# Kernel tuning notes

Hardware: AMD Instinct MI355X
Metric: run time of the kernel (lower is better)

Reference implementation:

```python
import math
import jax, jax.numpy as jnp
import numpy as np

HEAD_SIZE = 64
MAX_LEN = 1024
ENT_HEADS = 2
REL_HEADS = 24
NEG_BIG = 1e12


def rope_tables(max_pos=MAX_LEN, head_size=HEAD_SIZE):
    # coord_dim=2 -> table built with d_hid = head_size // 2
    d = head_size // 2
    pos = jnp.arange(max_pos, dtype=jnp.float32)[:, None]            # [P,1]
    div = jnp.exp(jnp.arange(0, d, 2, dtype=jnp.float32) * (-math.log(10000.0) / d))  # [d/2]
    ang = pos * div                                                   # [P, d/2]
    # table[:,1::2]=cos, table[:,::2]=sin; repeat_interleave(2) == jnp.repeat(...,2)
    cosp = jnp.repeat(jnp.cos(ang), 2, axis=-1)                       # [P, d]
    sinp = jnp.repeat(jnp.sin(ang), 2, axis=-1)                       # [P, d]
    return cosp, sinp


def apply_rope2d(qw, cosp, sinp, xp, yp):
    # qw: [b,s,h,hs]; xp,yp: [b,s] int positions
    cos = jnp.concatenate([cosp[xp], cosp[yp]], axis=-1)[:, :, None, :]  # [b,s,1,hs]
    sin = jnp.concatenate([sinp[xp], sinp[yp]], axis=-1)[:, :, None, :]
    qw2 = jnp.stack([-qw[..., 1::2], qw[..., ::2]], axis=-1).reshape(qw.shape)
    return qw * cos + qw2 * sin


def gp_layer(x, W, b, heads, mask, xp, yp, cosp, sinp, tril):
    hs = HEAD_SIZE
    bsz, s, _ = x.shape
    # dense then torch.chunk(heads)+stack == reshape to [b,s,heads,2*hs]
    seq = (x @ W + b).reshape(bsz, s, heads, 2 * hs)
    qw, kw = seq[..., :hs], seq[..., hs:]
    qw = apply_rope2d(qw, cosp, sinp, xp, yp)
    kw = apply_rope2d(kw, cosp, sinp, xp, yp)
    logits = jnp.einsum('bmhd,bnhd->bhmn', qw, kw)                    # [b,h,s,s]
    pad = (mask[:, None, :, None] > 0) & (mask[:, None, None, :] > 0)
    logits = jnp.where(pad, logits, -jnp.inf)
    if tril:
        logits = logits - jnp.tril(jnp.ones((s, s), logits.dtype), -1) * NEG_BIG
    return logits / (hs ** 0.5)


def setup_inputs() -> dict:
    key = jax.random.key(0)
    ks = jax.random.split(key, 8)
    b, s, h = 4, 512, 1024
    return {
        'last_hidden_state': jax.random.normal(ks[0], (b, s, h), dtype=jnp.float32),
        'attention_mask': jnp.ones((b, s), dtype=jnp.int32),
        'x_pos': jax.random.randint(ks[1], (b, s), 0, MAX_LEN, dtype=jnp.int32),
        'y_pos': jax.random.randint(ks[2], (b, s), 0, MAX_LEN, dtype=jnp.int32),
        'W_ent': jax.random.normal(ks[3], (h, ENT_HEADS * 2 * HEAD_SIZE), dtype=jnp.float32) * 0.02,
        'b_ent': jnp.zeros((ENT_HEADS * 2 * HEAD_SIZE,), dtype=jnp.float32),
        'W_head': jax.random.normal(ks[4], (h, REL_HEADS * 2 * HEAD_SIZE), dtype=jnp.float32) * 0.02,
        'b_head': jnp.zeros((REL_HEADS * 2 * HEAD_SIZE,), dtype=jnp.float32),
        'W_tail': jax.random.normal(ks[5], (h, REL_HEADS * 2 * HEAD_SIZE), dtype=jnp.float32) * 0.02,
        'b_tail': jnp.zeros((REL_HEADS * 2 * HEAD_SIZE,), dtype=jnp.float32),
    }


def reference(last_hidden_state, attention_mask, x_pos, y_pos,
              W_ent, b_ent, W_head, b_head, W_tail, b_tail):
    cosp, sinp = rope_tables()
    ent = gp_layer(last_hidden_state, W_ent, b_ent, ENT_HEADS,
                   attention_mask, x_pos, y_pos, cosp, sinp, tril=True)
    head = gp_layer(last_hidden_state, W_head, b_head, REL_HEADS,
                    attention_mask, x_pos, y_pos, cosp, sinp, tril=False)
    tail = gp_layer(last_hidden_state, W_tail, b_tail, REL_HEADS,
                    attention_mask, x_pos, y_pos, cosp, sinp, tril=False)
    return jnp.concatenate([ent, head, tail], axis=1)  # [b, 2+24+24, s, s]
```

## Files before the change

### kernel.cpp

```cpp
#include <hip/hip_runtime.h>
#include <hip/hip_bf16.h>
#include <math.h>

#define NUM_B 4
#define SEQ 512
#define HID 1024
#define NH 50
#define NCOL 6400
#define M_TOK 2048

typedef short bf16x8_t __attribute__((ext_vector_type(8)));
typedef float f32x4_t __attribute__((ext_vector_type(4)));

__device__ __forceinline__ unsigned short f2bf(float f) {
    union { float f; unsigned int u; } v; v.f = f;
    unsigned int u = v.u;
    u += 0x7fffu + ((u >> 16) & 1u);
    return (unsigned short)(u >> 16);
}

__device__ __forceinline__ void gload_lds16(const void* g, void* l) {
    __builtin_amdgcn_global_load_lds(
        (__attribute__((address_space(1))) unsigned int*)(unsigned long long)g,
        (__attribute__((address_space(3))) unsigned int*)(unsigned long long)(uintptr_t)l,
        16, 0, 0);
}

__global__ void k_prep(const float* __restrict__ x, unsigned short* __restrict__ xb,
                       float2* __restrict__ csT,
                       const float* __restrict__ be, const float* __restrict__ bh,
                       const float* __restrict__ bt, float* __restrict__ ball) {
    int bid = blockIdx.x, tid = threadIdx.x;
    if (bid < 2048) {
        int i = bid * 256 + tid;
        float4 v = ((const float4*)x)[i];
        ushort4 o;
        o.x = f2bf(v.x); o.y = f2bf(v.y); o.z = f2bf(v.z); o.w = f2bf(v.w);
        ((ushort4*)xb)[i] = o;
    } else if (bid < 2112) {
        int idx = (bid - 2048) * 256 + tid;
        int p = idx >> 4, t2 = idx & 15;
        float ang = (float)p * expf(-logf(10000.f) * (float)(2 * t2) / 32.f);
        csT[idx] = make_float2(cosf(ang), sinf(ang));
    } else {
        int i = (bid - 2112) * 256 + tid;
        if (i < 6400) {
            float v;
            if (i < 256) v = be[i];
            else if (i < 3328) v = bh[i - 256];
            else v = bt[i - 3328];
            ball[i] = v;
        }
    }
}

__global__ void k_cvt_w(const float* __restrict__ We, const float* __restrict__ Wh,
                        const float* __restrict__ Wl, unsigned short* __restrict__ Wo) {
    __shared__ float t[32][33];
    int n = blockIdx.x * 32 + threadIdx.x;
    const float* W; int Nw, nc;
    if (n < 256)       { W = We; Nw = 256;  nc = n; }
    else if (n < 3328) { W = Wh; Nw = 3072; nc = n - 256; }
    else               { W = Wl; Nw = 3072; nc = n - 3328; }
    int k = blockIdx.y * 32 + threadIdx.y;
    t[threadIdx.y][threadIdx.x] = W[(size_t)k * Nw + nc];
    __syncthreads();
    int on = blockIdx.x * 32 + threadIdx.y;
    int ok = blockIdx.y * 32 + threadIdx.x;
    Wo[(size_t)on * HID + ok] = f2bf(t[threadIdx.x][threadIdx.y]);
}

#define FUSED_LDS_BYTES (144 * 1024)

__global__ __launch_bounds__(512, 2) void k_fused(const unsigned short* __restrict__ xb,
                                                  const unsigned short* __restrict__ Wt,
                                                  const float* __restrict__ bias,
                                                  const int* __restrict__ xp,
                                                  const int* __restrict__ yp,
                                                  const float2* __restrict__ csT,
                                                  const int* __restrict__ mask,
                                                  float* __restrict__ out) {
    extern __shared__ unsigned short smem[];
    unsigned short* As = smem;
    unsigned short* Bs = smem + 512 * 64;
    unsigned short* Qs = smem;
    unsigned short* Ks = smem + 640 * 64;

    int tid = threadIdx.x;
    int wave = tid >> 6, lane = tid & 63;
    int l15 = lane & 15, q = lane >> 4;
    int bh = blockIdx.x;
    int b = bh / NH, h = bh - b * NH;

    const unsigned short* Ab = xb + (size_t)b * SEQ * HID;
    const unsigned short* Bb = Wt + (size_t)h * 128 * HID;

    f32x4_t acc[8][4];
#pragma unroll
    for (int i = 0; i < 8; i++)
#pragma unroll
        for (int j = 0; j < 4; j++) acc[i][j] = (f32x4_t){0.f, 0.f, 0.f, 0.f};

    int wmg = (wave >> 1) * 128;
    int wqk = wave & 1;

    for (int k0 = 0; k0 < HID; k0 += 64) {
        __syncthreads();
#pragma unroll
        for (int it = 0; it < 8; ++it) {
            int c = it * 512 + tid;
            int r = c >> 3, cl = c & 7;
            int cg = cl ^ (r & 7);
            gload_lds16(Ab + (size_t)r * HID + k0 + cg * 8, As + c * 8);
        }
#pragma unroll
        for (int it = 0; it < 2; ++it) {
            int c = it * 512 + tid;
            int r = c >> 3, cl = c & 7;
            int cg = cl ^ (r & 7);
            gload_lds16(Bb + (size_t)r * HID + k0 + cg * 8, Bs + c * 8);
        }
        __syncthreads();
#pragma unroll
        for (int ks = 0; ks < 2; ++ks) {
            bf16x8_t af[8], bfr[4];
#pragma unroll
            for (int i = 0; i < 8; i++) {
                int r = wmg + i * 16 + l15;
                int cl = (ks * 4 + q) ^ (r & 7);
                af[i] = *(const bf16x8_t*)&As[r * 64 + cl * 8];
            }
#pragma unroll
            for (int j = 0; j < 4; j++) {
                int r = wqk * 64 + j * 16 + l15;
                int cl = (ks * 4 + q) ^ (r & 7);
                bfr[j] = *(const bf16x8_t*)&Bs[r * 64 + cl * 8];
            }
#pragma unroll
            for (int i = 0; i < 8; i++)
#pragma unroll
                for (int j = 0; j < 4; j++)
                    acc[i][j] = __builtin_amdgcn_mfma_f32_16x16x32_bf16(bfr[j], af[i], acc[i][j], 0, 0, 0);
        }
    }

    __syncthreads();

    float4 bj[4];
#pragma unroll
    for (int j = 0; j < 4; j++)
        bj[j] = *(const float4*)&bias[h * 128 + wqk * 64 + j * 16 + q * 4];
    unsigned short* dst = wqk ? Ks : Qs;
#pragma unroll
    for (int i = 0; i < 8; i++) {
        int m = wmg + i * 16 + l15;
        int mg = b * SEQ + m;
        int posx = xp[mg] * 16, posy = yp[mg] * 16;
#pragma unroll
        for (int j = 0; j < 4; j++) {
            float v0 = acc[i][j][0] + bj[j].x;
            float v1 = acc[i][j][1] + bj[j].y;
            float v2 = acc[i][j][2] + bj[j].z;
            float v3 = acc[i][j][3] + bj[j].w;
            int pos = (j < 2) ? posx : posy;
            int t2 = (j & 1) * 8 + q * 2;
            float2 cs0 = csT[pos + t2];
            float2 cs1 = csT[pos + t2 + 1];
            float r0 = v0 * cs0.x - v1 * cs0.y;
            float r1 = v1 * cs0.x + v0 * cs0.y;
            float r2 = v2 * cs1.x - v3 * cs1.y;
            float r3 = v3 * cs1.x + v2 * cs1.y;
            ushort4 o;
            o.x = f2bf(r0); o.y = f2bf(r1); o.z = f2bf(r2); o.w = f2bf(r3);
            int cl0 = j * 2 + (q >> 1);
            int swz = cl0 ^ (m & 7);
            *(ushort4*)&dst[m * 64 + swz * 8 + (q & 1) * 4] = o;
        }
    }
    __syncthreads();

    bf16x8_t qf[4][2];
#pragma unroll
    for (int i = 0; i < 4; i++) {
        int r = wave * 64 + i * 16 + l15;
#pragma unroll
        for (int ks = 0; ks < 2; ks++) {
            int cl = (ks * 4 + q) ^ (r & 7);
            qf[i][ks] = *(const bf16x8_t*)&Qs[r * 64 + cl * 8];
        }
    }

    const int* mrow = mask + b * SEQ;
    bool enth = (h < 2);
    size_t obase = (size_t)bh * SEQ * SEQ;
    int mloc[4]; bool mz[4];
#pragma unroll
    for (int i = 0; i < 4; i++) {
        mloc[i] = wave * 64 + i * 16 + l15;
        mz[i] = (mrow[mloc[i]] == 0);
    }

    for (int nc = 0; nc < 8; ++nc) {
        bf16x8_t kf[4][2];
#pragma unroll
        for (int j = 0; j < 4; j++) {
            int r = nc * 64 + j * 16 + l15;
#pragma unroll
            for (int ks = 0; ks < 2; ks++) {
                int cl = (ks * 4 + q) ^ (r & 7);
                kf[j][ks] = *(const bf16x8_t*)&Ks[r * 64 + cl * 8];
            }
        }
        f32x4_t a2[4][4];
#pragma unroll
        for (int i = 0; i < 4; i++)
#pragma unroll
            for (int j = 0; j < 4; j++) a2[i][j] = (f32x4_t){0.f, 0.f, 0.f, 0.f};
#pragma unroll
        for (int ks = 0; ks < 2; ks++)
#pragma unroll
            for (int i = 0; i < 4; i++)
#pragma unroll
                for (int j = 0; j < 4; j++)
                    a2[i][j] = __builtin_amdgcn_mfma_f32_16x16x32_bf16(kf[j][ks], qf[i][ks], a2[i][j], 0, 0, 0);

        int4 mn[4];
#pragma unroll
        for (int j = 0; j < 4; j++)
            mn[j] = *(const int4*)&mrow[nc * 64 + j * 16 + q * 4];
#pragma unroll
        for (int i = 0; i < 4; i++) {
            int m = mloc[i];
#pragma unroll
            for (int j = 0; j < 4; j++) {
                int nb = nc * 64 + j * 16 + q * 4;
                float4 v;
                v.x = a2[i][j][0] * 0.125f;
                v.y = a2[i][j][1] * 0.125f;
                v.z = a2[i][j][2] * 0.125f;
                v.w = a2[i][j][3] * 0.125f;
                if (enth) {
                    if (m > nb)     v.x -= 1.25e11f;
                    if (m > nb + 1) v.y -= 1.25e11f;
                    if (m > nb + 2) v.z -= 1.25e11f;
                    if (m > nb + 3) v.w -= 1.25e11f;
                }
                if (mz[i] || mn[j].x == 0) v.x = -INFINITY;
                if (mz[i] || mn[j].y == 0) v.y = -INFINITY;
                if (mz[i] || mn[j].z == 0) v.z = -INFINITY;
                if (mz[i] || mn[j].w == 0) v.w = -INFINITY;
                *(float4*)&out[obase + (size_t)m * SEQ + nb] = v;
            }
        }
    }
}

extern "C" void kernel_launch(void* const* d_in, const int* in_sizes, int n_in,
                              void* d_out, int out_size, void* d_ws, size_t ws_size,
                              hipStream_t stream) {
    const float* x      = (const float*)d_in[0];
    const int*   mask   = (const int*)d_in[1];
    const int*   xp     = (const int*)d_in[2];
    const int*   yp     = (const int*)d_in[3];
    const float* W_ent  = (const float*)d_in[4];
    const float* b_ent  = (const float*)d_in[5];
    const float* W_head = (const float*)d_in[6];
    const float* b_head = (const float*)d_in[7];
    const float* W_tail = (const float*)d_in[8];
    const float* b_tail = (const float*)d_in[9];
    float* out = (float*)d_out;

    char* ws = (char*)d_ws;
    size_t off = 0;
    auto alloc = [&](size_t bytes) {
        void* p = ws + off;
        off += (bytes + 255) & ~(size_t)255;
        return p;
    };
    float2* csT = (float2*)alloc(16384 * 8);
    unsigned short* xb  = (unsigned short*)alloc((size_t)M_TOK * HID * 2);
    unsigned short* Wt  = (unsigned short*)alloc((size_t)NCOL * HID * 2);
    float* ball = (float*)alloc(NCOL * 4);

    static bool attr_done = false;
    if (!attr_done) {
        (void)hipFuncSetAttribute((const void*)k_fused,
                                  hipFuncAttributeMaxDynamicSharedMemorySize,
                                  FUSED_LDS_BYTES);
        attr_done = true;
    }

    k_prep<<<2137, 256, 0, stream>>>(x, xb, csT, b_ent, b_head, b_tail, ball);
    k_cvt_w<<<dim3(200, 32), dim3(32, 32), 0, stream>>>(W_ent, W_head, W_tail, Wt);
    k_fused<<<NUM_B * NH, 512, FUSED_LDS_BYTES, stream>>>(xb, Wt, ball, xp, yp, csT, mask, out);
}
```

Before: 308.0 us.

## Double-buffer projection GEMM tiles and use 1024-thread blocks for fused kernel

The fused kernel now runs 16 waves per block instead of 8. The projection GEMM stages its K-tiles into two LDS buffers, so the global-to-LDS load for the next tile overlaps the MFMA work on the current one. Each wave's accumulator tile is halved, and the QK^T output phase splits the key columns between wave pairs. LDS grows to 160KB and the launch bounds change, which adds per-block barrier cost, may allow only one block per CU, and raises register pressure at 1024 threads.

Result: no change. 308.7 us (+0.2%).

```diff
diff --git a/kernel.cpp b/kernel.cpp
--- a/kernel.cpp
+++ b/kernel.cpp
@@ -70,19 +70,17 @@
     Wo[(size_t)on * HID + ok] = f2bf(t[threadIdx.x][threadIdx.y]);
 }
 
-#define FUSED_LDS_BYTES (144 * 1024)
-
-__global__ __launch_bounds__(512, 2) void k_fused(const unsigned short* __restrict__ xb,
-                                                  const unsigned short* __restrict__ Wt,
-                                                  const float* __restrict__ bias,
-                                                  const int* __restrict__ xp,
-                                                  const int* __restrict__ yp,
-                                                  const float2* __restrict__ csT,
-                                                  const int* __restrict__ mask,
-                                                  float* __restrict__ out) {
+#define FUSED_LDS_BYTES (160 * 1024)
+
+__global__ __launch_bounds__(1024, 4) void k_fused(const unsigned short* __restrict__ xb,
+                                                   const unsigned short* __restrict__ Wt,
+                                                   const float* __restrict__ bias,
+                                                   const int* __restrict__ xp,
+                                                   const int* __restrict__ yp,
+                                                   const float2* __restrict__ csT,
+                                                   const int* __restrict__ mask,
+                                                   float* __restrict__ out) {
     extern __shared__ unsigned short smem[];
-    unsigned short* As = smem;
-    unsigned short* Bs = smem + 512 * 64;
     unsigned short* Qs = smem;
     unsigned short* Ks = smem + 640 * 64;
 
@@ -95,56 +93,63 @@
     const unsigned short* Ab = xb + (size_t)b * SEQ * HID;
     const unsigned short* Bb = Wt + (size_t)h * 128 * HID;
 
-    f32x4_t acc[8][4];
-#pragma unroll
-    for (int i = 0; i < 8; i++)
-#pragma unroll
-        for (int j = 0; j < 4; j++) acc[i][j] = (f32x4_t){0.f, 0.f, 0.f, 0.f};
-
-    int wmg = (wave >> 1) * 128;
+    int wmg = (wave >> 1) * 64;
     int wqk = wave & 1;
 
-    for (int k0 = 0; k0 < HID; k0 += 64) {
-        __syncthreads();
-#pragma unroll
-        for (int it = 0; it < 8; ++it) {
-            int c = it * 512 + tid;
+    auto stage = [&](int buf, int k0) {
+        unsigned short* As_ = smem + buf * 40960;
+        unsigned short* Bs_ = As_ + 512 * 64;
+#pragma unroll
+        for (int it = 0; it < 4; ++it) {
+            int c = it * 1024 + tid;
             int r = c >> 3, cl = c & 7;
             int cg = cl ^ (r & 7);
-            gload_lds16(Ab + (size_t)r * HID + k0 + cg * 8, As + c * 8);
-        }
-#pragma unroll
-        for (int it = 0; it < 2; ++it) {
-            int c = it * 512 + tid;
+            gload_lds16(Ab + (size_t)r * HID + k0 + cg * 8, As_ + c * 8);
+        }
+        {
+            int c = tid;
             int r = c >> 3, cl = c & 7;
             int cg = cl ^ (r & 7);
-            gload_lds16(Bb + (size_t)r * HID + k0 + cg * 8, Bs + c * 8);
-        }
-        __syncthreads();
+            gload_lds16(Bb + (size_t)r * HID + k0 + cg * 8, Bs_ + c * 8);
+        }
+    };
+
+    f32x4_t acc[4][4];
+#pragma unroll
+    for (int i = 0; i < 4; i++)
+#pragma unroll
+        for (int j = 0; j < 4; j++) acc[i][j] = (f32x4_t){0.f, 0.f, 0.f, 0.f};
+
+    stage(0, 0);
+    __syncthreads();
+    for (int t = 0; t < 16; ++t) {
+        int cur = t & 1;
+        if (t < 15) stage(cur ^ 1, (t + 1) * 64);
+        const unsigned short* As_ = smem + cur * 40960;
+        const unsigned short* Bs_ = As_ + 512 * 64;
 #pragma unroll
         for (int ks = 0; ks < 2; ++ks) {
-            bf16x8_t af[8], bfr[4];
-#pragma unroll
-            for (int i = 0; i < 8; i++) {
+            bf16x8_t af[4], bfr[4];
+#pragma unroll
+            for (int i = 0; i < 4; i++) {
                 int r = wmg + i * 16 + l15;
                 int cl = (ks * 4 + q) ^ (r & 7);
-                af[i] = *(const bf16x8_t*)&As[r * 64 + cl * 8];
+                af[i] = *(const bf16x8_t*)&As_[r * 64 + cl * 8];
             }
 #pragma unroll
             for (int j = 0; j < 4; j++) {
                 int r = wqk * 64 + j * 16 + l15;
                 int cl = (ks * 4 + q) ^ (r & 7);
-                bfr[j] = *(const bf16x8_t*)&Bs[r * 64 + cl * 8];
+                bfr[j] = *(const bf16x8_t*)&Bs_[r * 64 + cl * 8];
             }
 #pragma unroll
-            for (int i = 0; i < 8; i++)
+            for (int i = 0; i < 4; i++)
 #pragma unroll
                 for (int j = 0; j < 4; j++)
                     acc[i][j] = __builtin_amdgcn_mfma_f32_16x16x32_bf16(bfr[j], af[i], acc[i][j], 0, 0, 0);
         }
-    }
-
-    __syncthreads();
+        __syncthreads();
+    }
 
     float4 bj[4];
 #pragma unroll
@@ -152,7 +157,7 @@
         bj[j] = *(const float4*)&bias[h * 128 + wqk * 64 + j * 16 + q * 4];
     unsigned short* dst = wqk ? Ks : Qs;
 #pragma unroll
-    for (int i = 0; i < 8; i++) {
+    for (int i = 0; i < 4; i++) {
         int m = wmg + i * 16 + l15;
         int mg = b * SEQ + m;
         int posx = xp[mg] * 16, posy = yp[mg] * 16;
@@ -182,7 +187,7 @@
     bf16x8_t qf[4][2];
 #pragma unroll
     for (int i = 0; i < 4; i++) {
-        int r = wave * 64 + i * 16 + l15;
+        int r = wmg + i * 16 + l15;
 #pragma unroll
         for (int ks = 0; ks < 2; ks++) {
             int cl = (ks * 4 + q) ^ (r & 7);
@@ -196,60 +201,65 @@
     int mloc[4]; bool mz[4];
 #pragma unroll
     for (int i = 0; i < 4; i++) {
-        mloc[i] = wave * 64 + i * 16 + l15;
+        mloc[i] = wmg + i * 16 + l15;
         mz[i] = (mrow[mloc[i]] == 0);
     }
-
-    for (int nc = 0; nc < 8; ++nc) {
-        bf16x8_t kf[4][2];
-#pragma unroll
-        for (int j = 0; j < 4; j++) {
-            int r = nc * 64 + j * 16 + l15;
-#pragma unroll
-            for (int ks = 0; ks < 2; ks++) {
-                int cl = (ks * 4 + q) ^ (r & 7);
-                kf[j][ks] = *(const bf16x8_t*)&Ks[r * 64 + cl * 8];
+    int nhalf = wave & 1;
+
+    for (int c4 = 0; c4 < 4; ++c4) {
+        int nc = nhalf * 4 + c4;
+#pragma unroll
+        for (int jb = 0; jb < 2; ++jb) {
+            bf16x8_t kf[2][2];
+#pragma unroll
+            for (int jj = 0; jj < 2; ++jj) {
+                int r = nc * 64 + (jb * 2 + jj) * 16 + l15;
+#pragma unroll
+                for (int ks = 0; ks < 2; ks++) {
+                    int cl = (ks * 4 + q) ^ (r & 7);
+                    kf[jj][ks] = *(const bf16x8_t*)&Ks[r * 64 + cl * 8];
+                }
             }
-        }
-        f32x4_t a2[4][4];
-#pragma unroll
-        for (int i = 0; i < 4; i++)
-#pragma unroll
-            for (int j = 0; j < 4; j++) a2[i][j] = (f32x4_t){0.f, 0.f, 0.f, 0.f};
-#pragma unroll
-        for (int ks = 0; ks < 2; ks++)
+            f32x4_t a2[4][2];
 #pragma unroll
             for (int i = 0; i < 4; i++)
 #pragma unroll
-                for (int j = 0; j < 4; j++)
-                    a2[i][j] = __builtin_amdgcn_mfma_f32_16x16x32_bf16(kf[j][ks], qf[i][ks], a2[i][j], 0, 0, 0);
-
-        int4 mn[4];
-#pragma unroll
-        for (int j = 0; j < 4; j++)
-            mn[j] = *(const int4*)&mrow[nc * 64 + j * 16 + q * 4];
-#pragma unroll
-        for (int i = 0; i < 4; i++) {
-            int m = mloc[i];
-#pragma unroll
-            for (int j = 0; j < 4; j++) {
-                int nb = nc * 64 + j * 16 + q * 4;
-                float4 v;
-                v.x = a2[i][j][0] * 0.125f;
-                v.y = a2[i][j][1] * 0.125f;
-                v.z = a2[i][j][2] * 0.125f;
-                v.w = a2[i][j][3] * 0.125f;
-                if (enth) {
-                    if (m > nb)     v.x -= 1.25e11f;
-                    if (m > nb + 1) v.y -= 1.25e11f;
-                    if (m > nb + 2) v.z -= 1.25e11f;
-                    if (m > nb + 3) v.w -= 1.25e11f;
+                for (int jj = 0; jj < 2; jj++) a2[i][jj] = (f32x4_t){0.f, 0.f, 0.f, 0.f};
+#pragma unroll
+            for (int ks = 0; ks < 2; ks++)
+#pragma unroll
+                for (int i = 0; i < 4; i++)
+#pragma unroll
+                    for (int jj = 0; jj < 2; jj++)
+                        a2[i][jj] = __builtin_amdgcn_mfma_f32_16x16x32_bf16(kf[jj][ks], qf[i][ks], a2[i][jj], 0, 0, 0);
+
+            int4 mn[2];
+#pragma unroll
+            for (int jj = 0; jj < 2; jj++)
+                mn[jj] = *(const int4*)&mrow[nc * 64 + (jb * 2 + jj) * 16 + q * 4];
+#pragma unroll
+            for (int i = 0; i < 4; i++) {
+                int m = mloc[i];
+#pragma unroll
+                for (int jj = 0; jj < 2; jj++) {
+                    int nb = nc * 64 + (jb * 2 + jj) * 16 + q * 4;
+                    float4 v;
+                    v.x = a2[i][jj][0] * 0.125f;
+                    v.y = a2[i][jj][1] * 0.125f;
+                    v.z = a2[i][jj][2] * 0.125f;
+                    v.w = a2[i][jj][3] * 0.125f;
+                    if (enth) {
+                        if (m > nb)     v.x -= 1.25e11f;
+                        if (m > nb + 1) v.y -= 1.25e11f;
+                        if (m > nb + 2) v.z -= 1.25e11f;
+                        if (m > nb + 3) v.w -= 1.25e11f;
+                    }
+                    if (mz[i] || mn[jj].x == 0) v.x = -INFINITY;
+                    if (mz[i] || mn[jj].y == 0) v.y = -INFINITY;
+                    if (mz[i] || mn[jj].z == 0) v.z = -INFINITY;
+                    if (mz[i] || mn[jj].w == 0) v.w = -INFINITY;
+                    *(float4*)&out[obase + (size_t)m * SEQ + nb] = v;
                 }
-                if (mz[i] || mn[j].x == 0) v.x = -INFINITY;
-                if (mz[i] || mn[j].y == 0) v.y = -INFINITY;
-                if (mz[i] || mn[j].z == 0) v.z = -INFINITY;
-                if (mz[i] || mn[j].w == 0) v.w = -INFINITY;
-                *(float4*)&out[obase + (size_t)m * SEQ + nb] = v;
             }
         }
     }
@@ -292,5 +302,5 @@
 
     k_prep<<<2137, 256, 0, stream>>>(x, xb, csT, b_ent, b_head, b_tail, ball);
     k_cvt_w<<<dim3(200, 32), dim3(32, 32), 0, stream>>>(W_ent, W_head, W_tail, Wt);
-    k_fused<<<NUM_B * NH, 512, FUSED_LDS_BYTES, stream>>>(xb, Wt, ball, xp, yp, csT, mask, out);
-}
+    k_fused<<<NUM_B * NH, 1024, FUSED_LDS_BYTES, stream>>>(xb, Wt, ball, xp, yp, csT, mask, out);
+}
```
